# Kernel optimization log

Hardware: AMD Instinct MI355X
Metric: run time of the kernel (lower is better)

Reference implementation:

```python
import jax, jax.numpy as jnp
import numpy as np

T_STEPS = 1000
TEMP_SAMPLE = 0.1


def _cosine_schedule():
    # matches MBDDegradationImputation._cosine_beta_schedule (float64 then cast)
    s = 0.008
    x = np.linspace(0, T_STEPS, T_STEPS + 1, dtype=np.float64)
    ac = np.cos((x / T_STEPS + s) / (1 + s) * np.pi * 0.5) ** 2
    ac = ac / ac[0]
    betas = np.clip(1.0 - ac[1:] / ac[:-1], 0.0, 0.999)
    alphas = 1.0 - betas
    acp = np.cumprod(alphas)
    return (jnp.asarray(alphas, jnp.float32),
            jnp.asarray(acp, jnp.float32),
            jnp.asarray(np.sqrt(1.0 - acp), jnp.float32))


def setup_inputs() -> dict:
    key = jax.random.key(0)
    k = jax.random.split(key, 6)
    N, T, F = 2048, 512, 64
    Xbar_i = jax.random.normal(k[0], (T, F), jnp.float32)
    observed_data = jax.random.normal(k[1], (T, F), jnp.float32)
    time_points = jnp.linspace(0.0, 1.0, T, dtype=jnp.float32)
    mask = jax.random.uniform(k[2], (T, F)) > 0.3  # True = observed
    eps = jax.random.normal(k[3], (N, T, F), jnp.float32)
    deg_a = jax.random.normal(k[4], (F,), jnp.float32) * 0.1
    deg_b = jax.random.normal(k[5], (F,), jnp.float32) * 0.1
    return {"Xbar_i": Xbar_i, "observed_data": observed_data,
            "time_points": time_points, "mask": mask, "eps": eps,
            "deg_a": deg_a, "deg_b": deg_b, "i": 500}


def reference(Xbar_i, observed_data, time_points, mask, eps, deg_a, deg_b, i):
    alphas, acp, sigmas = _cosine_schedule()
    abar_i = acp[i]
    sigma_i = sigmas[i]
    alpha_i = alphas[i]
    abar_im1 = acp[i - 1]

    Yi = jnp.sqrt(abar_i) * Xbar_i  # (T, F)
    # candidate clean samples, clipped, observed positions restored
    X0s = jnp.clip(eps * sigma_i + Xbar_i, -1.0, 1.0)  # (N, T, F)
    cand = jnp.where(mask[None], observed_data[None], X0s)  # (N, T, F)

    # linear degradation model consistency: pred = a + b * t, score = -MSE
    pred = deg_a[None, :] + deg_b[None, :] * time_points[:, None]  # (T, F)
    scores = -jnp.mean((cand - pred[None]) ** 2, axis=(1, 2))  # (N,)

    std = jnp.maximum(jnp.std(scores, ddof=1), 1e-4)  # torch.std is unbiased
    logp0 = (scores - jnp.mean(scores)) / std / TEMP_SAMPLE
    weights = jax.nn.softmax(logp0)  # (N,)

    weighted = jnp.einsum('n,ntf->tf', weights, X0s)  # (T, F)
    # per-feature: missing positions get weighted combo; fully-observed
    # features are copied from observed_data; observed positions of
    # partially-missing features stay zero (faithful to the torch loop)
    feat_all = jnp.all(mask, axis=0)  # (F,)
    Xbar = jnp.where(~mask, weighted,
                     jnp.where(feat_all[None, :], observed_data, 0.0))

    score = (-Yi + jnp.sqrt(abar_i) * Xbar) / (1.0 - abar_i)
    Xim1 = (Yi + (1.0 - abar_i) * score) / jnp.sqrt(alpha_i)
    Xbar_im1 = Xim1 / jnp.sqrt(abar_im1)
    Xbar_im1 = jnp.where(mask, observed_data, Xbar_im1)
    return Xbar_im1
```

## Files before the change

kernel.cpp:

```cpp
#include <hip/hip_runtime.h>

typedef __attribute__((ext_vector_type(4))) int   i32x4;
typedef __attribute__((ext_vector_type(4))) float f32x4;

#define TF    32768
#define TF4   8192
#define NS    2048
#define ROWS  8
#define NG    32
#define WCUT  1e-9f

__device__ __forceinline__ i32x4 mload4(const void* mask, int isI32, int idx4) {
  if (isI32) return ((const i32x4*)mask)[idx4];
  unsigned int w = ((const unsigned int*)mask)[idx4];
  i32x4 r;
  r[0] = (int)(w & 0xFFu);
  r[1] = (int)((w >> 8) & 0xFFu);
  r[2] = (int)((w >> 16) & 0xFFu);
  r[3] = (int)((w >> 24) & 0xFFu);
  return r;
}

__device__ __forceinline__ double ac_fn(int t) {
  const double s = 0.008;
  double c = cos(((double)t / 1000.0 + s) / (1.0 + s) * 1.5707963267948966);
  return c * c;
}
__device__ __forceinline__ double alpha_fn(int t) {
  double beta = 1.0 - ac_fn(t + 1) / ac_fn(t);
  beta = beta < 0.0 ? 0.0 : (beta > 0.999 ? 0.999 : beta);
  return 1.0 - beta;
}

__launch_bounds__(256, 4)
__global__ void k12_scores(const int* __restrict__ ip,
                           const unsigned int* __restrict__ maskw,
                           const float* __restrict__ timep,
                           const float* __restrict__ dega,
                           const float* __restrict__ degb,
                           const float* __restrict__ xbar,
                           const float* __restrict__ obs,
                           const void* __restrict__ mask,
                           const float* __restrict__ eps,
                           float* __restrict__ wsc,
                           double* __restrict__ pscore) {
  const int tid = threadIdx.x;
  __shared__ double red[ROWS * 256];
  __shared__ int badsh;
  __shared__ float ssig;
  __shared__ int sIsI32;

  if (tid == 0) badsh = 0;
  __syncthreads();
  int bad = 0;
  for (int k = tid; k < TF4; k += 256)
    if (maskw[k] > 1u) bad = 1;
  if (bad) atomicOr(&badsh, 1);

  const int i = ip[0];
  double p = 1.0;
  for (int t = tid; t < i; t += 256) p *= alpha_fn(t);
  red[tid] = p;
  __syncthreads();
  for (int s = 128; s > 0; s >>= 1) {
    if (tid < s) red[tid] *= red[tid + s];
    __syncthreads();
  }
  if (tid == 0) {
    double acp_im1 = red[0];
    double ai = alpha_fn(i);
    double acp_i = acp_im1 * ai;
    float sig = (float)sqrt(1.0 - acp_i);
    ssig = sig;
    sIsI32 = badsh ? 0 : 1;
    if (blockIdx.x == 0 && blockIdx.y == 0) {
      wsc[0] = sig;
      wsc[1] = (float)acp_i;
      wsc[2] = (float)ai;
      wsc[3] = (float)acp_im1;
      ((int*)wsc)[8] = badsh ? 0 : 1;
    }
  }
  __syncthreads();
  const float sig = ssig;
  const int isI32 = sIsI32;

  const int n0 = blockIdx.x * ROWS;
  const int kq = blockIdx.y;
  const int kbeg = kq * (TF4 / 4);
  const f32x4* e4 = (const f32x4*)eps;
  const f32x4* x4 = (const f32x4*)xbar;
  const f32x4* o4 = (const f32x4*)obs;

  double acc[ROWS];
  #pragma unroll
  for (int r = 0; r < ROWS; ++r) acc[r] = 0.0;

  #pragma unroll 2
  for (int k = kbeg + tid; k < kbeg + TF4 / 4; k += 256) {
    f32x4 x = x4[k], o = o4[k];
    i32x4 m = mload4(mask, isI32, k);
    const int t  = k >> 4;
    const int f0 = (k << 2) & 63;
    const float tv = timep[t];
    f32x4 da = *(const f32x4*)(dega + f0);
    f32x4 db = *(const f32x4*)(degb + f0);
    f32x4 sv, xv, pv;
    #pragma unroll
    for (int c = 0; c < 4; ++c) {
      const float pr = fmaf(db[c], tv, da[c]);
      const bool mm = m[c] != 0;
      sv[c] = mm ? 0.f : sig;
      xv[c] = mm ? 0.f : x[c];
      pv[c] = mm ? (o[c] - pr) : pr;
    }
    #pragma unroll
    for (int r = 0; r < ROWS; ++r) {
      f32x4 e = e4[(size_t)(n0 + r) * TF4 + k];
      float s = 0.f;
      #pragma unroll
      for (int c = 0; c < 4; ++c) {
        float v = fmaf(e[c], sv[c], xv[c]);
        v = fminf(fmaxf(v, -1.f), 1.f);
        float d = v - pv[c];
        s = fmaf(d, d, s);
      }
      acc[r] += (double)s;
    }
  }
  #pragma unroll
  for (int r = 0; r < ROWS; ++r) red[r * 256 + tid] = acc[r];
  __syncthreads();
  for (int s = 128; s > 0; s >>= 1) {
    if (tid < s) {
      #pragma unroll
      for (int r = 0; r < ROWS; ++r) red[r * 256 + tid] += red[r * 256 + tid + s];
    }
    __syncthreads();
  }
  if (tid < ROWS) pscore[kq * NS + n0 + tid] = red[tid * 256];
}

__launch_bounds__(256)
__global__ void k34_weighted(const double* __restrict__ pscore,
                             const float* __restrict__ eps,
                             const float* __restrict__ xbar,
                             const float* __restrict__ wsc,
                             float* __restrict__ partial) {
  const int tid = threadIdx.x;
  __shared__ double red[256];
  __shared__ int cnt[256];
  __shared__ int   ciL[NS];
  __shared__ float cwL[NS];

  float s[8];
  #pragma unroll
  for (int j = 0; j < 8; ++j) {
    int n = tid + 256 * j;
    double t = pscore[n] + pscore[NS + n] + pscore[2 * NS + n] + pscore[3 * NS + n];
    s[j] = -(float)(t * (1.0 / 32768.0));
  }
  double t = 0.0;
  #pragma unroll
  for (int j = 0; j < 8; ++j) t += (double)s[j];
  red[tid] = t; __syncthreads();
  for (int st = 128; st > 0; st >>= 1) { if (tid < st) red[tid] += red[tid + st]; __syncthreads(); }
  const float mean = (float)(red[0] * (1.0 / 2048.0));
  __syncthreads();
  double v = 0.0;
  #pragma unroll
  for (int j = 0; j < 8; ++j) { float d = s[j] - mean; v += (double)d * (double)d; }
  red[tid] = v; __syncthreads();
  for (int st = 128; st > 0; st >>= 1) { if (tid < st) red[tid] += red[tid + st]; __syncthreads(); }
  float stdv = (float)sqrt(red[0] / 2047.0);
  stdv = fmaxf(stdv, 1e-4f);
  const float inv = 10.0f / stdv;
  float lp[8];
  double mx = -1e300;
  #pragma unroll
  for (int j = 0; j < 8; ++j) { lp[j] = (s[j] - mean) * inv; mx = fmax(mx, (double)lp[j]); }
  __syncthreads();
  red[tid] = mx; __syncthreads();
  for (int st = 128; st > 0; st >>= 1) { if (tid < st) red[tid] = fmax(red[tid], red[tid + st]); __syncthreads(); }
  const float M = (float)red[0];
  __syncthreads();
  float ev[8]; double es = 0.0;
  #pragma unroll
  for (int j = 0; j < 8; ++j) { ev[j] = expf(lp[j] - M); es += (double)ev[j]; }
  red[tid] = es; __syncthreads();
  for (int st = 128; st > 0; st >>= 1) { if (tid < st) red[tid] += red[tid + st]; __syncthreads(); }
  const float invS = (float)(1.0 / red[0]);

  float w[8]; int keep[8]; int c = 0;
  #pragma unroll
  for (int j = 0; j < 8; ++j) {
    w[j] = ev[j] * invS;
    keep[j] = w[j] > WCUT;
    c += keep[j];
  }
  cnt[tid] = c; __syncthreads();
  for (int off = 1; off < 256; off <<= 1) {
    int vv = (tid >= off) ? cnt[tid - off] : 0;
    __syncthreads();
    cnt[tid] += vv;
    __syncthreads();
  }
  int base = cnt[tid] - c;
  #pragma unroll
  for (int j = 0; j < 8; ++j) {
    if (keep[j]) {
      ciL[base] = tid + 256 * j;
      cwL[base] = w[j];
      ++base;
    }
  }
  const int Nk = cnt[255];
  __syncthreads();

  const int pos4 = blockIdx.x * 256 + tid;
  const int g = blockIdx.y;
  const float sig = wsc[0];
  const f32x4* e4 = (const f32x4*)eps;
  f32x4 xf = ((const f32x4*)xbar)[pos4];
  f32x4 acc = {0.f, 0.f, 0.f, 0.f};
  int j = g;
  for (; j + NG < Nk; j += 2 * NG) {
    const float w0 = cwL[j];
    const int   n0 = ciL[j];
    const float w1 = cwL[j + NG];
    const int   n1 = ciL[j + NG];
    f32x4 e0 = e4[(size_t)n0 * TF4 + pos4];
    f32x4 e1 = e4[(size_t)n1 * TF4 + pos4];
    #pragma unroll
    for (int c2 = 0; c2 < 4; ++c2) {
      float vv = fmaf(e0[c2], sig, xf[c2]);
      vv = fminf(fmaxf(vv, -1.f), 1.f);
      acc[c2] = fmaf(w0, vv, acc[c2]);
    }
    #pragma unroll
    for (int c2 = 0; c2 < 4; ++c2) {
      float vv = fmaf(e1[c2], sig, xf[c2]);
      vv = fminf(fmaxf(vv, -1.f), 1.f);
      acc[c2] = fmaf(w1, vv, acc[c2]);
    }
  }
  for (; j < Nk; j += NG) {
    const float ww = cwL[j];
    const int n = ciL[j];
    f32x4 e = e4[(size_t)n * TF4 + pos4];
    #pragma unroll
    for (int c2 = 0; c2 < 4; ++c2) {
      float vv = fmaf(e[c2], sig, xf[c2]);
      vv = fminf(fmaxf(vv, -1.f), 1.f);
      acc[c2] = fmaf(ww, vv, acc[c2]);
    }
  }
  ((f32x4*)partial)[(size_t)g * TF4 + pos4] = acc;
}

__launch_bounds__(256)
__global__ void k5_final(const float* __restrict__ partial,
                         const float* __restrict__ xbar,
                         const float* __restrict__ obs,
                         const void* __restrict__ mask,
                         const float* __restrict__ wsc,
                         float* __restrict__ out) {
  const int pos4 = blockIdx.x * 256 + threadIdx.x;
  const f32x4* p4 = (const f32x4*)partial;
  f32x4 w = {0.f, 0.f, 0.f, 0.f};
  #pragma unroll 8
  for (int g = 0; g < NG; ++g) {
    f32x4 a = p4[(size_t)g * TF4 + pos4];
    #pragma unroll
    for (int c = 0; c < 4; ++c) w[c] += a[c];
  }
  const float abar = wsc[1];
  const float sa = sqrtf(abar);
  const float ra = 1.f / sqrtf(wsc[2]);
  const float rb = 1.f / sqrtf(wsc[3]);
  const int isI32 = ((const int*)wsc)[8];
  f32x4 xf = ((const f32x4*)xbar)[pos4];
  f32x4 ov = ((const f32x4*)obs)[pos4];
  i32x4 m = mload4(mask, isI32, pos4);
  f32x4 res;
  #pragma unroll
  for (int c = 0; c < 4; ++c) {
    const float Yi = sa * xf[c];
    const float scv = (-Yi + sa * w[c]) / (1.f - abar);
    const float xim1 = (Yi + (1.f - abar) * scv) * ra;
    res[c] = m[c] ? ov[c] : (xim1 * rb);
  }
  ((f32x4*)out)[pos4] = res;
}

extern "C" void kernel_launch(void* const* d_in, const int* in_sizes, int n_in,
                              void* d_out, int out_size, void* d_ws, size_t ws_size,
                              hipStream_t stream) {
  const float* Xbar  = (const float*)d_in[0];
  const float* obs   = (const float*)d_in[1];
  const float* timep = (const float*)d_in[2];
  const void*  mask  = d_in[3];
  const float* eps   = (const float*)d_in[4];
  const float* dega  = (const float*)d_in[5];
  const float* degb  = (const float*)d_in[6];
  const int*   ip    = (const int*)d_in[7];

  float* ws = (float*)d_ws;
  float*  wsc     = ws;
  double* pscore  = (double*)(ws + 16);
  float*  partial = (float*)(pscore + 4 * NS);

  hipLaunchKernelGGL(k12_scores, dim3(NS/ROWS, 4), dim3(256), 0, stream,
                     ip, (const unsigned int*)mask, timep, dega, degb,
                     Xbar, obs, mask, eps, wsc, pscore);
  hipLaunchKernelGGL(k34_weighted, dim3(32, NG),   dim3(256), 0, stream,
                     pscore, eps, Xbar, wsc, partial);
  hipLaunchKernelGGL(k5_final,     dim3(32),       dim3(256), 0, stream,
                     partial, Xbar, obs, mask, wsc, (float*)d_out);
}
```

Measured before the change: 73.30 us.

## Split score kernel into precomputed mask/pred tables and lean streaming pass

Adds a small pre-kernel that computes the schedule constants, the masked Xbar, the prediction/observed residual tables and a per-vector mask bitmask once. The main score kernel then streams eps against these tables instead of recomputing the schedule product, the mask check and the predictions in every block. The loop is also unrolled by two with independent loads, and the accumulators are now float instead of double. The cost is an extra kernel launch and small workspace tables, plus some precision loss from float accumulation.

```diff
diff --git a/kernel.cpp b/kernel.cpp
--- a/kernel.cpp
+++ b/kernel.cpp
@@ -32,24 +32,22 @@
   return 1.0 - beta;
 }
 
-__launch_bounds__(256, 4)
-__global__ void k12_scores(const int* __restrict__ ip,
-                           const unsigned int* __restrict__ maskw,
-                           const float* __restrict__ timep,
-                           const float* __restrict__ dega,
-                           const float* __restrict__ degb,
-                           const float* __restrict__ xbar,
-                           const float* __restrict__ obs,
-                           const void* __restrict__ mask,
-                           const float* __restrict__ eps,
-                           float* __restrict__ wsc,
-                           double* __restrict__ pscore) {
+__launch_bounds__(256)
+__global__ void k1_tables(const int* __restrict__ ip,
+                          const unsigned int* __restrict__ maskw,
+                          const float* __restrict__ timep,
+                          const float* __restrict__ dega,
+                          const float* __restrict__ degb,
+                          const float* __restrict__ xbar,
+                          const float* __restrict__ obs,
+                          const void* __restrict__ mask,
+                          float* __restrict__ wsc,
+                          float* __restrict__ xq, float* __restrict__ pq,
+                          unsigned char* __restrict__ bm) {
   const int tid = threadIdx.x;
-  __shared__ double red[ROWS * 256];
   __shared__ int badsh;
-  __shared__ float ssig;
+  __shared__ double prod[256];
   __shared__ int sIsI32;
-
   if (tid == 0) badsh = 0;
   __syncthreads();
   int bad = 0;
@@ -60,21 +58,19 @@
   const int i = ip[0];
   double p = 1.0;
   for (int t = tid; t < i; t += 256) p *= alpha_fn(t);
-  red[tid] = p;
+  prod[tid] = p;
   __syncthreads();
   for (int s = 128; s > 0; s >>= 1) {
-    if (tid < s) red[tid] *= red[tid + s];
+    if (tid < s) prod[tid] *= prod[tid + s];
     __syncthreads();
   }
   if (tid == 0) {
-    double acp_im1 = red[0];
-    double ai = alpha_fn(i);
-    double acp_i = acp_im1 * ai;
-    float sig = (float)sqrt(1.0 - acp_i);
-    ssig = sig;
     sIsI32 = badsh ? 0 : 1;
-    if (blockIdx.x == 0 && blockIdx.y == 0) {
-      wsc[0] = sig;
+    if (blockIdx.x == 0) {
+      double acp_im1 = prod[0];
+      double ai = alpha_fn(i);
+      double acp_i = acp_im1 * ai;
+      wsc[0] = (float)sqrt(1.0 - acp_i);
       wsc[1] = (float)acp_i;
       wsc[2] = (float)ai;
       wsc[3] = (float)acp_im1;
@@ -82,54 +78,90 @@
     }
   }
   __syncthreads();
-  const float sig = ssig;
   const int isI32 = sIsI32;
 
+  const int pos4 = blockIdx.x * 256 + tid;
+  const int t  = pos4 >> 4;
+  const int f0 = (pos4 << 2) & 63;
+  const float tv = timep[t];
+  f32x4 da = *(const f32x4*)(dega + f0);
+  f32x4 db = *(const f32x4*)(degb + f0);
+  f32x4 x  = ((const f32x4*)xbar)[pos4];
+  f32x4 o  = ((const f32x4*)obs)[pos4];
+  i32x4 m  = mload4(mask, isI32, pos4);
+
+  f32x4 xv, pv;
+  unsigned int bits = 0;
+  #pragma unroll
+  for (int c = 0; c < 4; ++c) {
+    const float pr = fmaf(db[c], tv, da[c]);
+    const bool mm = m[c] != 0;
+    bits |= mm ? (1u << c) : 0u;
+    xv[c] = mm ? 0.f : x[c];
+    pv[c] = mm ? (o[c] - pr) : pr;
+  }
+  ((f32x4*)xq)[pos4] = xv;
+  ((f32x4*)pq)[pos4] = pv;
+  bm[pos4] = (unsigned char)bits;
+}
+
+__launch_bounds__(256, 4)
+__global__ void k2_scores(const float* __restrict__ eps,
+                          const float* __restrict__ xq,
+                          const float* __restrict__ pq,
+                          const unsigned char* __restrict__ bm,
+                          const float* __restrict__ wsc,
+                          double* __restrict__ pscore) {
+  const int tid = threadIdx.x;
   const int n0 = blockIdx.x * ROWS;
   const int kq = blockIdx.y;
   const int kbeg = kq * (TF4 / 4);
+  const float sig = wsc[0];
   const f32x4* e4 = (const f32x4*)eps;
-  const f32x4* x4 = (const f32x4*)xbar;
-  const f32x4* o4 = (const f32x4*)obs;
-
-  double acc[ROWS];
-  #pragma unroll
-  for (int r = 0; r < ROWS; ++r) acc[r] = 0.0;
-
-  #pragma unroll 2
-  for (int k = kbeg + tid; k < kbeg + TF4 / 4; k += 256) {
-    f32x4 x = x4[k], o = o4[k];
-    i32x4 m = mload4(mask, isI32, k);
-    const int t  = k >> 4;
-    const int f0 = (k << 2) & 63;
-    const float tv = timep[t];
-    f32x4 da = *(const f32x4*)(dega + f0);
-    f32x4 db = *(const f32x4*)(degb + f0);
-    f32x4 sv, xv, pv;
+  const f32x4* xq4 = (const f32x4*)xq;
+  const f32x4* pq4 = (const f32x4*)pq;
+
+  float acc[ROWS];
+  #pragma unroll
+  for (int r = 0; r < ROWS; ++r) acc[r] = 0.f;
+
+  for (int k = kbeg + tid; k < kbeg + TF4 / 4; k += 512) {
+    const int k1 = k + 256;
+    f32x4 xv0 = xq4[k],  pv0 = pq4[k];
+    f32x4 xv1 = xq4[k1], pv1 = pq4[k1];
+    const unsigned int b0 = bm[k], b1 = bm[k1];
+    f32x4 sv0, sv1;
     #pragma unroll
     for (int c = 0; c < 4; ++c) {
-      const float pr = fmaf(db[c], tv, da[c]);
-      const bool mm = m[c] != 0;
-      sv[c] = mm ? 0.f : sig;
-      xv[c] = mm ? 0.f : x[c];
-      pv[c] = mm ? (o[c] - pr) : pr;
+      sv0[c] = (b0 & (1u << c)) ? 0.f : sig;
+      sv1[c] = (b1 & (1u << c)) ? 0.f : sig;
     }
     #pragma unroll
     for (int r = 0; r < ROWS; ++r) {
-      f32x4 e = e4[(size_t)(n0 + r) * TF4 + k];
+      const size_t row = (size_t)(n0 + r) * TF4;
+      f32x4 e0 = e4[row + k];
+      f32x4 e1 = e4[row + k1];
       float s = 0.f;
       #pragma unroll
       for (int c = 0; c < 4; ++c) {
-        float v = fmaf(e[c], sv[c], xv[c]);
+        float v = fmaf(e0[c], sv0[c], xv0[c]);
         v = fminf(fmaxf(v, -1.f), 1.f);
-        float d = v - pv[c];
+        float d = v - pv0[c];
         s = fmaf(d, d, s);
       }
-      acc[r] += (double)s;
-    }
-  }
-  #pragma unroll
-  for (int r = 0; r < ROWS; ++r) red[r * 256 + tid] = acc[r];
+      #pragma unroll
+      for (int c = 0; c < 4; ++c) {
+        float v = fmaf(e1[c], sv1[c], xv1[c]);
+        v = fminf(fmaxf(v, -1.f), 1.f);
+        float d = v - pv1[c];
+        s = fmaf(d, d, s);
+      }
+      acc[r] += s;
+    }
+  }
+  __shared__ double red[ROWS * 256];
+  #pragma unroll
+  for (int r = 0; r < ROWS; ++r) red[r * 256 + tid] = (double)acc[r];
   __syncthreads();
   for (int s = 128; s > 0; s >>= 1) {
     if (tid < s) {
@@ -307,12 +339,17 @@
 
   float* ws = (float*)d_ws;
   float*  wsc     = ws;
-  double* pscore  = (double*)(ws + 16);
+  float*  xq      = ws + 16;
+  float*  pq      = xq + TF;
+  unsigned char* bm = (unsigned char*)(pq + TF);
+  double* pscore  = (double*)(pq + TF + TF4/4);
   float*  partial = (float*)(pscore + 4 * NS);
 
-  hipLaunchKernelGGL(k12_scores, dim3(NS/ROWS, 4), dim3(256), 0, stream,
+  hipLaunchKernelGGL(k1_tables,  dim3(32),         dim3(256), 0, stream,
                      ip, (const unsigned int*)mask, timep, dega, degb,
-                     Xbar, obs, mask, eps, wsc, pscore);
+                     Xbar, obs, mask, wsc, xq, pq, bm);
+  hipLaunchKernelGGL(k2_scores,  dim3(NS/ROWS, 4), dim3(256), 0, stream,
+                     eps, xq, pq, bm, wsc, pscore);
   hipLaunchKernelGGL(k34_weighted, dim3(32, NG),   dim3(256), 0, stream,
                      pscore, eps, Xbar, wsc, partial);
   hipLaunchKernelGGL(k5_final,     dim3(32),       dim3(256), 0, stream,
```

New measurement: 76.91 us. +4.9%, slower.
